# Kernel tuning notes

Hardware: AMD Instinct MI355X
Metric: run time of the kernel (lower is better)

## Reference

```python
import jax, jax.numpy as jnp
import numpy as np

B, H, W, C, NH, WS, NB = 8, 64, 64, 384, 12, 8, 2
N = H * W
NWT = WS * WS  # tokens per window
SHIFT = WS // 2

def _rel_index(ws):
    coords = np.stack(np.meshgrid(np.arange(ws), np.arange(ws), indexing='ij')).reshape(2, -1)
    rel = (coords[:, :, None] - coords[:, None, :]).transpose(1, 2, 0)
    rel[..., 0] += ws - 1
    rel[..., 1] += ws - 1
    rel[..., 0] *= 2 * ws - 1
    return rel.sum(-1)  # (ws*ws, ws*ws)

REL_IDX = _rel_index(WS)

def _shift_mask(h, w, ws, shift):
    img = np.zeros((h, w))
    cnt = 0
    for hs in (slice(0, -ws), slice(-ws, -shift), slice(-shift, None)):
        for wsl in (slice(0, -ws), slice(-ws, -shift), slice(-shift, None)):
            img[hs, wsl] = cnt
            cnt += 1
    win = img.reshape(h // ws, ws, w // ws, ws).transpose(0, 2, 1, 3).reshape(-1, ws * ws)
    diff = win[:, None, :] - win[:, :, None]
    return np.where(diff != 0, -100.0, 0.0).astype(np.float32)  # (nW, NWT, NWT)

MASK = jnp.asarray(_shift_mask(H, W, WS, SHIFT))

def _ln(x, g, b, eps=1e-5):
    m = jnp.mean(x, -1, keepdims=True)
    v = jnp.mean((x - m) ** 2, -1, keepdims=True)
    return (x - m) * jax.lax.rsqrt(v + eps) * g + b

def _partition(x):
    b = x.shape[0]
    x = x.reshape(b, H // WS, WS, W // WS, WS, C).transpose(0, 1, 3, 2, 4, 5)
    return x.reshape(-1, NWT, C)

def _reverse(wx, b):
    x = wx.reshape(b, H // WS, W // WS, WS, WS, C).transpose(0, 1, 3, 2, 4, 5)
    return x.reshape(b, H, W, C)

def _attention(xw, qkv_w, qkv_b, proj_w, proj_b, rpb, mask):
    B_, Nt, Cc = xw.shape
    hd = Cc // NH
    qkv = (xw @ qkv_w + qkv_b).reshape(B_, Nt, 3, NH, hd).transpose(2, 0, 3, 1, 4)
    q, k, v = qkv[0], qkv[1], qkv[2]
    bias = rpb[REL_IDX].transpose(2, 0, 1)[None]  # (1, NH, Nt, Nt)
    attn = jnp.einsum('bhnd,bhmd->bhnm', q * (hd ** -0.5), k) + bias
    if mask is not None:
        nW = mask.shape[0]
        attn = attn.reshape(B_ // nW, nW, NH, Nt, Nt) + mask[None, :, None]
        attn = attn.reshape(B_, NH, Nt, Nt)
    attn = jax.nn.softmax(attn, axis=-1)
    out = jnp.einsum('bhnm,bhmd->bhnd', attn, v).transpose(0, 2, 1, 3).reshape(B_, Nt, Cc)
    return out @ proj_w + proj_b

def _swin_block(x, p, shift):
    n1g, n1b, n2g, n2b, qw, qb, pw, pb, w1, b1, w2, b2, rpb = p
    shortcut = x
    h = _ln(x, n1g, n1b)
    if shift > 0:
        h = jnp.roll(h, (-shift, -shift), axis=(1, 2))
    hw = _attention(_partition(h), qw, qb, pw, pb, rpb, MASK if shift > 0 else None)
    h = _reverse(hw, x.shape[0])
    if shift > 0:
        h = jnp.roll(h, (shift, shift), axis=(1, 2))
    x = shortcut + h
    h = _ln(x, n2g, n2b)
    h = jax.nn.gelu(h @ w1 + b1) @ w2 + b2
    return x + h


def setup_inputs() -> dict:
    key = jax.random.key(0)
    ks = jax.random.split(key, 6)
    s = 0.02
    return {
        'x': jax.random.normal(ks[0], (B, N, C), jnp.float32),
        'outer_g': jnp.ones((NB, C), jnp.float32),
        'outer_b': jnp.zeros((NB, C), jnp.float32),
        'n1_g': jnp.ones((NB, C), jnp.float32),
        'n1_b': jnp.zeros((NB, C), jnp.float32),
        'n2_g': jnp.ones((NB, C), jnp.float32),
        'n2_b': jnp.zeros((NB, C), jnp.float32),
        'qkv_w': jax.random.normal(ks[1], (NB, C, 3 * C), jnp.float32) * s,
        'qkv_b': jnp.zeros((NB, 3 * C), jnp.float32),
        'proj_w': jax.random.normal(ks[2], (NB, C, C), jnp.float32) * s,
        'proj_b': jnp.zeros((NB, C), jnp.float32),
        'mlp_w1': jax.random.normal(ks[3], (NB, C, 4 * C), jnp.float32) * s,
        'mlp_b1': jnp.zeros((NB, 4 * C), jnp.float32),
        'mlp_w2': jax.random.normal(ks[4], (NB, 4 * C, C), jnp.float32) * s,
        'mlp_b2': jnp.zeros((NB, C), jnp.float32),
        'rpb': jax.random.normal(ks[5], (NB, (2 * WS - 1) ** 2, NH), jnp.float32) * s,
    }


def reference(x, outer_g, outer_b, n1_g, n1_b, n2_g, n2_b, qkv_w, qkv_b, proj_w, proj_b, mlp_w1, mlp_b1, mlp_w2, mlp_b2, rpb):
    xv = x.reshape(B, H, W, C)
    for i in range(NB):
        shift = 0 if i % 2 == 0 else SHIFT
        p = (n1_g[i], n1_b[i], n2_g[i], n2_b[i], qkv_w[i], qkv_b[i], proj_w[i], proj_b[i],
             mlp_w1[i], mlp_b1[i], mlp_w2[i], mlp_b2[i], rpb[i])
        residual = xv
        xv = _swin_block(_ln(xv, outer_g[i], outer_b[i]), p, shift) + residual
    return xv.reshape(B, N, C)
```

## Files before the change

### kernel.cpp

```cpp
#include <hip/hip_runtime.h>
#include <hip/hip_bf16.h>

#define BATCH 8
#define HDIM 64
#define WDIM 64
#define CC 384
#define NHE 12
#define HD 32
#define NTOK 32768
#define NBLK 2

typedef short short8 __attribute__((ext_vector_type(8)));
typedef float f32x4 __attribute__((ext_vector_type(4)));

__device__ __forceinline__ float bf2f(unsigned short u) {
  return __uint_as_float(((unsigned int)u) << 16);
}
__device__ __forceinline__ unsigned short f2bf(float f) {
  __hip_bfloat16 h = __float2bfloat16(f);
  return *reinterpret_cast<unsigned short*>(&h);
}
__device__ __forceinline__ float wave_sum(float s) {
#pragma unroll
  for (int o = 32; o; o >>= 1) s += __shfl_xor(s, o, 64);
  return s;
}
__device__ __forceinline__ float gelu_f(float x) {
  float y = 0.7978845608028654f * (x + 0.044715f * x * x * x);
  float t = 1.0f - 2.0f / (__expf(2.0f * y) + 1.0f);
  return 0.5f * x * (1.0f + t);
}
__device__ __forceinline__ int regid(int x) {
  return x < 56 ? 0 : (x < 60 ? 1 : 2);
}
__device__ __forceinline__ void gload16(const void* g, void* l) {
  __builtin_amdgcn_global_load_lds(
      (const __attribute__((address_space(1))) unsigned int*)g,
      (__attribute__((address_space(3))) unsigned int*)l, 16, 0, 0);
}

__global__ __launch_bounds__(256) void wconv_kernel(
    const float* __restrict__ src, unsigned short* __restrict__ dst, int K, int N) {
  __shared__ float tile[64 * 65];
  const int bn = blockIdx.x * 64, bk = blockIdx.y * 64;
  const int t = threadIdx.x;
  const int lk = t >> 2, ln = (t & 3) * 16;
  const float* ps = src + (size_t)(bk + lk) * N + bn + ln;
#pragma unroll
  for (int j = 0; j < 4; ++j)
    *(float4*)&tile[lk * 65 + ln + 4 * j] = *(const float4*)(ps + 4 * j);
  __syncthreads();
  const int on = t >> 2, ok = (t & 3) * 16;
  unsigned short ob[16];
#pragma unroll
  for (int j = 0; j < 16; ++j) ob[j] = f2bf(tile[(ok + j) * 65 + on]);
  uint4* pd = (uint4*)(dst + (size_t)(bn + on) * K + bk + ok);
  pd[0] = ((const uint4*)ob)[0];
  pd[1] = ((const uint4*)ob)[1];
}

__global__ __launch_bounds__(256) void bias_prep_kernel(
    const float* __restrict__ rpb, float* __restrict__ biasT) {
  int idx = blockIdx.x * 256 + threadIdx.x;
  int m = idx & 63;
  int n = (idx >> 6) & 63;
  int h = idx >> 12;
  int dr = (n >> 3) - (m >> 3) + 7;
  int dc = (n & 7) - (m & 7) + 7;
  biasT[idx] = rpb[(dr * 15 + dc) * NHE + h];
}

__global__ __launch_bounds__(256) void ln_fused_kernel(
    const float* __restrict__ xin, const float* __restrict__ og,
    const float* __restrict__ ob, const float* __restrict__ n1g,
    const float* __restrict__ n1b, unsigned short* __restrict__ y0h,
    unsigned short* __restrict__ abuf, int shift) {
  const int lane = threadIdx.x & 63;
  const int token = blockIdx.x * 4 + (threadIdx.x >> 6);
  const float* px = xin + (size_t)token * CC;
  float v[6];
#pragma unroll
  for (int j = 0; j < 6; ++j) v[j] = px[j * 64 + lane];
  float s = 0.f;
#pragma unroll
  for (int j = 0; j < 6; ++j) s += v[j];
  s = wave_sum(s);
  float mean = s * (1.0f / CC);
  float q = 0.f;
#pragma unroll
  for (int j = 0; j < 6; ++j) { float d = v[j] - mean; q += d * d; }
  q = wave_sum(q);
  float rstd = rsqrtf(q * (1.0f / CC) + 1e-5f);
  unsigned short* py = y0h + (size_t)token * CC;
#pragma unroll
  for (int j = 0; j < 6; ++j) {
    int d = j * 64 + lane;
    float y = (v[j] - mean) * rstd * og[d] + ob[d];
    py[d] = f2bf(y);
    v[j] = y;
  }
  s = 0.f;
#pragma unroll
  for (int j = 0; j < 6; ++j) s += v[j];
  s = wave_sum(s);
  float mean2 = s * (1.0f / CC);
  q = 0.f;
#pragma unroll
  for (int j = 0; j < 6; ++j) { float d = v[j] - mean2; q += d * d; }
  q = wave_sum(q);
  float rstd2 = rsqrtf(q * (1.0f / CC) + 1e-5f);
  int b = token >> 12;
  int hh = (token >> 6) & 63;
  int ww = token & 63;
  int r = (hh - shift) & 63;
  int c = (ww - shift) & 63;
  int wrow = (((b << 6) + ((r >> 3) << 3) + (c >> 3)) << 6) + ((r & 7) << 3) + (c & 7);
  unsigned short* pa = abuf + (size_t)wrow * CC;
#pragma unroll
  for (int j = 0; j < 6; ++j) {
    int d = j * 64 + lane;
    pa[d] = f2bf((v[j] - mean2) * rstd2 * n1g[d] + n1b[d]);
  }
}

__global__ __launch_bounds__(256, 1) void apl_kernel(
    const unsigned short* __restrict__ qkv, const float* __restrict__ biasT,
    const unsigned short* __restrict__ y0h, const unsigned short* __restrict__ Btp,
    const float* __restrict__ pb, const float* __restrict__ g2,
    const float* __restrict__ b2, unsigned short* __restrict__ x1h,
    unsigned short* __restrict__ abuf, int shift) {
  __shared__ __align__(1024) char smem[65536];
  const int tid = threadIdx.x;
  const int wv = tid >> 6;
  const int lane = tid & 63;
  const int l0 = lane & 15;
  const int q = lane >> 4;
  const int wi = blockIdx.x;
  const int use_mask = (shift != 0);

  unsigned short* P16 = (unsigned short*)(smem + wv * 12288);
  unsigned short* Vt16 = (unsigned short*)(smem + wv * 12288 + 8192);
  float* Ol = (float*)(smem + wv * 12288);
  unsigned short* Obuf = (unsigned short*)(smem + 49152);

#define LDS_FENCE() asm volatile("s_waitcnt lgkmcnt(0)" ::: "memory")

  f32x4 pacc[4][6] = {};

  for (int p = 0; p < 3; ++p) {
    const int h = 4 * p + wv;
    const unsigned short* qbase = qkv + (size_t)(wi * 64) * 1152 + h * HD;
    short8 kf[4], qf[4];
#pragma unroll
    for (int mt = 0; mt < 4; ++mt)
      kf[mt] = *(const short8*)(qbase + (size_t)(16 * mt + l0) * 1152 + CC + 8 * q);
#pragma unroll
    for (int nt = 0; nt < 4; ++nt)
      qf[nt] = *(const short8*)(qbase + (size_t)(16 * nt + l0) * 1152 + 8 * q);

    f32x4 acc[4][4];
    const float* bh = biasT + h * 4096;
#pragma unroll
    for (int mt = 0; mt < 4; ++mt)
#pragma unroll
      for (int nt = 0; nt < 4; ++nt)
        acc[mt][nt] = *(const f32x4*)(bh + (l0 + 16 * nt) * 64 + 16 * mt + 4 * q);

    {
      unsigned short varr[32];
      const uint4* pv = (const uint4*)(qbase + (size_t)lane * 1152 + 2 * CC);
      uint4* t4 = (uint4*)varr;
      t4[0] = pv[0]; t4[1] = pv[1]; t4[2] = pv[2]; t4[3] = pv[3];
#pragma unroll
      for (int d = 0; d < 32; ++d)
        Vt16[d * 64 + 8 * ((lane >> 3) ^ (d & 7)) + (lane & 7)] = varr[d];
    }

    __builtin_amdgcn_s_setprio(1);
#pragma unroll
    for (int mt = 0; mt < 4; ++mt)
#pragma unroll
      for (int nt = 0; nt < 4; ++nt)
        acc[mt][nt] = __builtin_amdgcn_mfma_f32_16x16x32_bf16(kf[mt], qf[nt], acc[mt][nt], 0, 0, 0);
    __builtin_amdgcn_s_setprio(0);

    if (use_mask) {
      int wloc = wi & 63;
      int wy = (wloc >> 3) * 8, wx = (wloc & 7) * 8;
      int idn[4], idm[16];
#pragma unroll
      for (int nt = 0; nt < 4; ++nt) {
        int n = l0 + 16 * nt;
        idn[nt] = regid(wy + (n >> 3)) * 3 + regid(wx + (n & 7));
      }
#pragma unroll
      for (int mt = 0; mt < 4; ++mt)
#pragma unroll
        for (int r = 0; r < 4; ++r) {
          int m = 16 * mt + 4 * q + r;
          idm[mt * 4 + r] = regid(wy + (m >> 3)) * 3 + regid(wx + (m & 7));
        }
#pragma unroll
      for (int mt = 0; mt < 4; ++mt)
#pragma unroll
        for (int nt = 0; nt < 4; ++nt)
#pragma unroll
          for (int r = 0; r < 4; ++r)
            acc[mt][nt][r] += (idm[mt * 4 + r] == idn[nt]) ? 0.0f : -100.0f;
    }

    float inv[4];
#pragma unroll
    for (int nt = 0; nt < 4; ++nt) {
      float m0 = -1e30f;
#pragma unroll
      for (int mt = 0; mt < 4; ++mt)
#pragma unroll
        for (int r = 0; r < 4; ++r) m0 = fmaxf(m0, acc[mt][nt][r]);
      m0 = fmaxf(m0, __shfl_xor(m0, 16, 64));
      m0 = fmaxf(m0, __shfl_xor(m0, 32, 64));
      float s0 = 0.f;
#pragma unroll
      for (int mt = 0; mt < 4; ++mt)
#pragma unroll
        for (int r = 0; r < 4; ++r) {
          float e = __expf(acc[mt][nt][r] - m0);
          acc[mt][nt][r] = e;
          s0 += e;
        }
      s0 += __shfl_xor(s0, 16, 64);
      s0 += __shfl_xor(s0, 32, 64);
      inv[nt] = 1.0f / s0;
    }

#pragma unroll
    for (int mt = 0; mt < 4; ++mt)
#pragma unroll
      for (int nt = 0; nt < 4; ++nt) {
        unsigned int lo = (unsigned int)f2bf(acc[mt][nt][0] * inv[nt]) |
                          ((unsigned int)f2bf(acc[mt][nt][1] * inv[nt]) << 16);
        unsigned int hi = (unsigned int)f2bf(acc[mt][nt][2] * inv[nt]) |
                          ((unsigned int)f2bf(acc[mt][nt][3] * inv[nt]) << 16);
        unsigned int* dst = (unsigned int*)&P16[(l0 + 16 * nt) * 64 +
                                                8 * ((2 * mt + (q >> 1)) ^ (l0 & 7)) + 4 * (q & 1)];
        dst[0] = lo;
        dst[1] = hi;
      }
    LDS_FENCE();

    f32x4 oacc[4][2] = {};
    __builtin_amdgcn_s_setprio(1);
#pragma unroll
    for (int kt = 0; kt < 2; ++kt) {
      short8 pa[4], vb[2];
#pragma unroll
      for (int nt = 0; nt < 4; ++nt)
        pa[nt] = *(const short8*)&P16[(l0 + 16 * nt) * 64 + 8 * ((q + 4 * kt) ^ (l0 & 7))];
#pragma unroll
      for (int dt = 0; dt < 2; ++dt)
        vb[dt] = *(const short8*)&Vt16[(l0 + 16 * dt) * 64 + 8 * ((q + 4 * kt) ^ (l0 & 7))];
#pragma unroll
      for (int nt = 0; nt < 4; ++nt)
#pragma unroll
        for (int dt = 0; dt < 2; ++dt)
          oacc[nt][dt] = __builtin_amdgcn_mfma_f32_16x16x32_bf16(pa[nt], vb[dt], oacc[nt][dt], 0, 0, 0);
    }
    __builtin_amdgcn_s_setprio(0);
    LDS_FENCE();

#pragma unroll
    for (int nt = 0; nt < 4; ++nt)
#pragma unroll
      for (int dt = 0; dt < 2; ++dt)
#pragma unroll
        for (int r = 0; r < 4; ++r)
          Ol[(16 * nt + 4 * q + r) * 34 + l0 + 16 * dt] = oacc[nt][dt][r];
    LDS_FENCE();

    uint4 opack[4];
    int posv[4];
#pragma unroll
    for (int jj = 0; jj < 4; ++jj) {
      int c = 4 * wv + jj;
      posv[jj] = (c & 8) | ((c ^ lane) & 7);
      unsigned short tmp[8];
#pragma unroll
      for (int e = 0; e < 8; ++e) tmp[e] = f2bf(Ol[lane * 34 + jj * 8 + e]);
      opack[jj] = *(const uint4*)tmp;
    }
    __syncthreads();
#pragma unroll
    for (int jj = 0; jj < 4; ++jj)
      *(uint4*)&Obuf[lane * 128 + posv[jj] * 8] = opack[jj];
    __syncthreads();

#pragma unroll
    for (int kfl = 0; kfl < 4; ++kfl) {
      short8 a[4], b[6];
      int c2 = kfl * 4 + q;
      int pos2 = (c2 & 8) | ((c2 ^ l0) & 7);
#pragma unroll
      for (int mt = 0; mt < 4; ++mt)
        a[mt] = *(const short8*)&Obuf[(16 * mt + l0) * 128 + pos2 * 8];
#pragma unroll
      for (int nt = 0; nt < 6; ++nt)
        b[nt] = *(const short8*)(Btp + (size_t)(wv * 96 + nt * 16 + l0) * 384 +
                                 128 * p + 32 * kfl + 8 * q);
      __builtin_amdgcn_s_setprio(1);
#pragma unroll
      for (int mt = 0; mt < 4; ++mt)
#pragma unroll
        for (int nt = 0; nt < 6; ++nt)
          pacc[mt][nt] = __builtin_amdgcn_mfma_f32_16x16x32_bf16(a[mt], b[nt], pacc[mt][nt], 0, 0, 0);
      __builtin_amdgcn_s_setprio(0);
    }
  }
  __syncthreads();

  float pbv[6], g2v[6], b2v[6];
#pragma unroll
  for (int nt = 0; nt < 6; ++nt) {
    int col = wv * 96 + nt * 16 + l0;
    pbv[nt] = pb[col];
    g2v[nt] = g2[col];
    b2v[nt] = b2[col];
  }
  int dstrow[4][4];
#pragma unroll
  for (int mt = 0; mt < 4; ++mt)
#pragma unroll
    for (int rr = 0; rr < 4; ++rr) {
      int m = 16 * mt + 4 * q + rr;
      int grow = wi * 64 + m;
      int b_ = grow >> 12;
      int wl = (grow >> 6) & 63;
      int t = grow & 63;
      int rs = ((wl >> 3) << 3) + (t >> 3);
      int cs = ((wl & 7) << 3) + (t & 7);
      int hh = (rs + shift) & 63;
      int ww = (cs + shift) & 63;
      dstrow[mt][rr] = (((b_ << 6) + hh) << 6) + ww;
    }
#pragma unroll
  for (int mt = 0; mt < 4; ++mt)
#pragma unroll
    for (int nt = 0; nt < 6; ++nt)
#pragma unroll
      for (int rr = 0; rr < 4; ++rr) {
        size_t dst = (size_t)dstrow[mt][rr] * CC + wv * 96 + nt * 16 + l0;
        pacc[mt][nt][rr] += pbv[nt] + bf2f(y0h[dst]);
      }
  float* part = (float*)(smem + 49152);
  float* stats = (float*)(smem + 49152 + 2048);
#pragma unroll
  for (int mt = 0; mt < 4; ++mt)
#pragma unroll
    for (int rr = 0; rr < 4; ++rr) {
      float s = 0.f, ss = 0.f;
#pragma unroll
      for (int nt = 0; nt < 6; ++nt) {
        float v = pacc[mt][nt][rr];
        s += v;
        ss += v * v;
      }
#pragma unroll
      for (int o = 8; o; o >>= 1) {
        s += __shfl_xor(s, o, 64);
        ss += __shfl_xor(ss, o, 64);
      }
      if (l0 == 0) {
        int m = 16 * mt + 4 * q + rr;
        part[(m * 4 + wv) * 2] = s;
        part[(m * 4 + wv) * 2 + 1] = ss;
      }
    }
  __syncthreads();
  if (tid < 64) {
    float s = 0.f, ss = 0.f;
#pragma unroll
    for (int w = 0; w < 4; ++w) {
      s += part[(tid * 4 + w) * 2];
      ss += part[(tid * 4 + w) * 2 + 1];
    }
    float mean = s * (1.0f / CC);
    float var = ss * (1.0f / CC) - mean * mean;
    stats[tid * 2] = mean;
    stats[tid * 2 + 1] = rsqrtf(var + 1e-5f);
  }
  __syncthreads();
#pragma unroll
  for (int mt = 0; mt < 4; ++mt)
#pragma unroll
    for (int rr = 0; rr < 4; ++rr) {
      int m = 16 * mt + 4 * q + rr;
      float mean = stats[m * 2];
      float rstd = stats[m * 2 + 1];
#pragma unroll
      for (int nt = 0; nt < 6; ++nt) {
        float v = pacc[mt][nt][rr];
        size_t dst = (size_t)dstrow[mt][rr] * CC + wv * 96 + nt * 16 + l0;
        x1h[dst] = f2bf(v);
        abuf[dst] = f2bf((v - mean) * rstd * g2v[nt] + b2v[nt]);
      }
    }
#undef LDS_FENCE
}

template <int EPI, int NN, int KK>
__global__ __launch_bounds__(256, 2) void gemm_kernel(
    const unsigned short* __restrict__ A, const unsigned short* __restrict__ Bt,
    const float* __restrict__ bias, float* __restrict__ outf,
    unsigned short* __restrict__ outb, const unsigned short* __restrict__ add0h,
    const float* __restrict__ add1f) {
  __shared__ __align__(1024) char smem[65536];
  const int tid = threadIdx.x;
  const int lane = tid & 63;
  const int wv = tid >> 6;
  const int wm = wv & 1, wn = wv >> 1;
  const int rowBase = blockIdx.y * 128;
  const int colBase = blockIdx.x * 128;
  const int srow = lane >> 3;
  const int schunk = (lane & 7) ^ srow;
  const unsigned short* pA = A + (size_t)(rowBase + srow) * KK + 8 * schunk;
  const unsigned short* pB = Bt + (size_t)(colBase + srow) * KK + 8 * schunk;
  const int l0 = lane & 15;
  const int q = lane >> 4;
  f32x4 acc[4][4] = {};

#pragma unroll
  for (int i = 0; i < 4; ++i) {
    int c = i * 4 + wv;
    gload16(pA + (size_t)(8 * c) * KK, smem + c * 1024);
    gload16(pB + (size_t)(8 * c) * KK, smem + 16384 + c * 1024);
  }

#pragma unroll 2
  for (int k0 = 0; k0 < KK; k0 += 64) {
    const int cur = (k0 >> 6) & 1;
    char* curb = smem + cur * 32768;
    if (k0 + 64 < KK) {
      char* nxtb = smem + (cur ^ 1) * 32768;
#pragma unroll
      for (int i = 0; i < 4; ++i) {
        int c = i * 4 + wv;
        gload16(pA + (size_t)(8 * c) * KK + k0 + 64, nxtb + c * 1024);
        gload16(pB + (size_t)(8 * c) * KK + k0 + 64, nxtb + 16384 + c * 1024);
      }
      asm volatile("s_waitcnt vmcnt(8)" ::: "memory");
    } else {
      asm volatile("s_waitcnt vmcnt(0)" ::: "memory");
    }
    __builtin_amdgcn_s_barrier();
    const unsigned short* As = (const unsigned short*)curb;
    const unsigned short* Bs = (const unsigned short*)(curb + 16384);
#pragma unroll
    for (int ksub = 0; ksub < 2; ++ksub) {
      const int sc = ksub * 4 + q;
      short8 af[4], bfr[4];
#pragma unroll
      for (int im = 0; im < 4; ++im) {
        int r = wm * 64 + im * 16 + l0;
        af[im] = *(const short8*)&As[r * 64 + 8 * (sc ^ (r & 7))];
      }
#pragma unroll
      for (int in_ = 0; in_ < 4; ++in_) {
        int r = wn * 64 + in_ * 16 + l0;
        bfr[in_] = *(const short8*)&Bs[r * 64 + 8 * (sc ^ (r & 7))];
      }
      __builtin_amdgcn_s_setprio(1);
#pragma unroll
      for (int im = 0; im < 4; ++im)
#pragma unroll
        for (int in_ = 0; in_ < 4; ++in_)
          acc[im][in_] = __builtin_amdgcn_mfma_f32_16x16x32_bf16(
              af[im], bfr[in_], acc[im][in_], 0, 0, 0);
      __builtin_amdgcn_s_setprio(0);
    }
    __builtin_amdgcn_s_barrier();
  }
  const int quad = lane >> 4;
  const int lc = lane & 15;
#pragma unroll
  for (int im = 0; im < 4; ++im) {
    int rb = rowBase + wm * 64 + im * 16 + quad * 4;
#pragma unroll
    for (int in_ = 0; in_ < 4; ++in_) {
      int gcol = colBase + wn * 64 + in_ * 16 + lc;
      float bv = bias[gcol];
#pragma unroll
      for (int r = 0; r < 4; ++r) {
        int grow = rb + r;
        float v = acc[im][in_][r] + bv;
        if (EPI == 0) {
          if (gcol < CC) v *= 0.17677669529663687f;
          outb[(size_t)grow * NN + gcol] = f2bf(v);
        } else if (EPI == 1) {
          outb[(size_t)grow * NN + gcol] = f2bf(gelu_f(v));
        } else {
          size_t dst = (size_t)grow * CC + gcol;
          outf[dst] = bf2f(add0h[dst]) + add1f[dst] + v;
        }
      }
    }
  }
}

extern "C" void kernel_launch(void* const* d_in, const int* in_sizes, int n_in,
                              void* d_out, int out_size, void* d_ws, size_t ws_size,
                              hipStream_t stream) {
  const float* x    = (const float*)d_in[0];
  const float* og   = (const float*)d_in[1];
  const float* ob   = (const float*)d_in[2];
  const float* n1g  = (const float*)d_in[3];
  const float* n1b  = (const float*)d_in[4];
  const float* n2g  = (const float*)d_in[5];
  const float* n2b  = (const float*)d_in[6];
  const float* qkvw = (const float*)d_in[7];
  const float* qkvb = (const float*)d_in[8];
  const float* pw   = (const float*)d_in[9];
  const float* pb   = (const float*)d_in[10];
  const float* w1   = (const float*)d_in[11];
  const float* b1   = (const float*)d_in[12];
  const float* w2   = (const float*)d_in[13];
  const float* b2   = (const float*)d_in[14];
  const float* rpb  = (const float*)d_in[15];
  float* out = (float*)d_out;

  char* ws = (char*)d_ws;
  unsigned short* y0h   = (unsigned short*)(ws);
  unsigned short* x1h   = (unsigned short*)(ws + 25165824);
  unsigned short* a_bf  = (unsigned short*)(ws + 50331648);
  unsigned short* big_bf= (unsigned short*)(ws + 100663296);
  unsigned short* wt    = (unsigned short*)(ws + 201326592);
  float* biasT          = (float*)(ws + 100663296 + 75497472);

  for (int i = 0; i < NBLK; ++i) {
    unsigned short* wq = wt + (size_t)i * 1769472;
    wconv_kernel<<<dim3(18, 6), 256, 0, stream>>>(qkvw + (size_t)i * 442368, wq, 384, 1152);
    wconv_kernel<<<dim3(6, 6), 256, 0, stream>>>(pw + (size_t)i * 147456, wq + 442368, 384, 384);
    wconv_kernel<<<dim3(24, 6), 256, 0, stream>>>(w1 + (size_t)i * 589824, wq + 589824, 384, 1536);
    wconv_kernel<<<dim3(6, 24), 256, 0, stream>>>(w2 + (size_t)i * 589824, wq + 1179648, 1536, 384);
  }

  for (int i = 0; i < NBLK; ++i) {
    const float* xin = (i == 0) ? x : out;
    int shift = (i & 1) ? 4 : 0;
    unsigned short* wq = wt + (size_t)i * 1769472;
    ln_fused_kernel<<<8192, 256, 0, stream>>>(xin, og + i * 384, ob + i * 384,
                                              n1g + i * 384, n1b + i * 384, y0h, a_bf, shift);
    gemm_kernel<0, 1152, 384><<<dim3(9, 256), 256, 0, stream>>>(
        a_bf, wq, qkvb + i * 1152, nullptr, big_bf, nullptr, nullptr);
    bias_prep_kernel<<<192, 256, 0, stream>>>(rpb + i * 2700, biasT);
    apl_kernel<<<512, 256, 0, stream>>>(big_bf, biasT, y0h, wq + 442368,
                                        pb + i * 384, n2g + i * 384, n2b + i * 384,
                                        x1h, a_bf, shift);
    gemm_kernel<1, 1536, 384><<<dim3(12, 256), 256, 0, stream>>>(
        a_bf, wq + 589824, b1 + i * 1536, nullptr, big_bf, nullptr, nullptr);
    gemm_kernel<3, 384, 1536><<<dim3(3, 256), 256, 0, stream>>>(
        big_bf, wq + 1179648, b2 + i * 384, out, nullptr, x1h, xin);
  }
}
```

Measured before the change: 704.8 us.

## Merge weight conversion launches and prefetch next head's QKV in attention kernel

Replaces eight small weight-conversion launches with a single kernel that works out which matrix and tile each block handles. In the fused attention/projection kernel, K, Q and V fragments for the next head group are loaded into registers while the current one computes. Barriers become an explicit lgkmcnt wait plus s_barrier instead of __syncthreads. The aim is to hide global load latency and cut launch overhead, at the cost of extra register pressure that may lower occupancy.

```diff
diff --git a/kernel.cpp b/kernel.cpp
--- a/kernel.cpp
+++ b/kernel.cpp
@@ -39,18 +39,31 @@
       (__attribute__((address_space(3))) unsigned int*)l, 16, 0, 0);
 }
 
-__global__ __launch_bounds__(256) void wconv_kernel(
-    const float* __restrict__ src, unsigned short* __restrict__ dst, int K, int N) {
+__global__ __launch_bounds__(256) void wconv_all_kernel(
+    const float* __restrict__ qkvw, const float* __restrict__ pw,
+    const float* __restrict__ w1, const float* __restrict__ w2,
+    unsigned short* __restrict__ wt) {
+  int t = blockIdx.x;
+  const int i = t / 432;
+  t -= i * 432;
+  unsigned short* wq = wt + (size_t)i * 1769472;
+  const float* src;
+  unsigned short* dst;
+  int K, N, nx;
+  if (t < 108)      { src = qkvw + (size_t)i * 442368; dst = wq;           K = 384;  N = 1152; nx = 18; }
+  else if (t < 144) { t -= 108; src = pw + (size_t)i * 147456; dst = wq + 442368;  K = 384;  N = 384;  nx = 6; }
+  else if (t < 288) { t -= 144; src = w1 + (size_t)i * 589824; dst = wq + 589824;  K = 384;  N = 1536; nx = 24; }
+  else              { t -= 288; src = w2 + (size_t)i * 589824; dst = wq + 1179648; K = 1536; N = 384;  nx = 6; }
+  const int bn = (t % nx) * 64, bk = (t / nx) * 64;
   __shared__ float tile[64 * 65];
-  const int bn = blockIdx.x * 64, bk = blockIdx.y * 64;
-  const int t = threadIdx.x;
-  const int lk = t >> 2, ln = (t & 3) * 16;
+  const int tt = threadIdx.x;
+  const int lk = tt >> 2, ln = (tt & 3) * 16;
   const float* ps = src + (size_t)(bk + lk) * N + bn + ln;
 #pragma unroll
   for (int j = 0; j < 4; ++j)
     *(float4*)&tile[lk * 65 + ln + 4 * j] = *(const float4*)(ps + 4 * j);
   __syncthreads();
-  const int on = t >> 2, ok = (t & 3) * 16;
+  const int on = tt >> 2, ok = (tt & 3) * 16;
   unsigned short ob[16];
 #pragma unroll
   for (int j = 0; j < 16; ++j) ob[j] = f2bf(tile[(ok + j) * 65 + on]);
@@ -144,19 +157,34 @@
   unsigned short* Obuf = (unsigned short*)(smem + 49152);
 
 #define LDS_FENCE() asm volatile("s_waitcnt lgkmcnt(0)" ::: "memory")
+#define LDS_BARRIER() do { LDS_FENCE(); __builtin_amdgcn_s_barrier(); } while (0)
+
+#define LOADP(PP, KD, QD, VD)                                                          \
+  {                                                                                    \
+    const unsigned short* qb_ = qkv + (size_t)(wi * 64) * 1152 + (4 * (PP) + wv) * HD; \
+    _Pragma("unroll") for (int mt_ = 0; mt_ < 4; ++mt_)                                \
+        KD[mt_] = *(const short8*)(qb_ + (size_t)(16 * mt_ + l0) * 1152 + CC + 8 * q); \
+    _Pragma("unroll") for (int nt_ = 0; nt_ < 4; ++nt_)                                \
+        QD[nt_] = *(const short8*)(qb_ + (size_t)(16 * nt_ + l0) * 1152 + 8 * q);      \
+    const uint4* pv_ = (const uint4*)(qb_ + (size_t)lane * 1152 + 2 * CC);             \
+    VD[0] = pv_[0]; VD[1] = pv_[1]; VD[2] = pv_[2]; VD[3] = pv_[3];                    \
+  }
 
   f32x4 pacc[4][6] = {};
+
+  short8 kf[4], qf[4];
+  uint4 varr4[4];
+  LOADP(0, kf, qf, varr4);
 
   for (int p = 0; p < 3; ++p) {
     const int h = 4 * p + wv;
-    const unsigned short* qbase = qkv + (size_t)(wi * 64) * 1152 + h * HD;
-    short8 kf[4], qf[4];
-#pragma unroll
-    for (int mt = 0; mt < 4; ++mt)
-      kf[mt] = *(const short8*)(qbase + (size_t)(16 * mt + l0) * 1152 + CC + 8 * q);
-#pragma unroll
-    for (int nt = 0; nt < 4; ++nt)
-      qf[nt] = *(const short8*)(qbase + (size_t)(16 * nt + l0) * 1152 + 8 * q);
+
+    {
+      const unsigned short* varr = (const unsigned short*)varr4;
+#pragma unroll
+      for (int d = 0; d < 32; ++d)
+        Vt16[d * 64 + 8 * ((lane >> 3) ^ (d & 7)) + (lane & 7)] = varr[d];
+    }
 
     f32x4 acc[4][4];
     const float* bh = biasT + h * 4096;
@@ -166,15 +194,9 @@
       for (int nt = 0; nt < 4; ++nt)
         acc[mt][nt] = *(const f32x4*)(bh + (l0 + 16 * nt) * 64 + 16 * mt + 4 * q);
 
-    {
-      unsigned short varr[32];
-      const uint4* pv = (const uint4*)(qbase + (size_t)lane * 1152 + 2 * CC);
-      uint4* t4 = (uint4*)varr;
-      t4[0] = pv[0]; t4[1] = pv[1]; t4[2] = pv[2]; t4[3] = pv[3];
-#pragma unroll
-      for (int d = 0; d < 32; ++d)
-        Vt16[d * 64 + 8 * ((lane >> 3) ^ (d & 7)) + (lane & 7)] = varr[d];
-    }
+    short8 kfn[4], qfn[4];
+    uint4 varrn[4];
+    if (p < 2) { LOADP(p + 1, kfn, qfn, varrn); }
 
     __builtin_amdgcn_s_setprio(1);
 #pragma unroll
@@ -288,11 +310,11 @@
       for (int e = 0; e < 8; ++e) tmp[e] = f2bf(Ol[lane * 34 + jj * 8 + e]);
       opack[jj] = *(const uint4*)tmp;
     }
-    __syncthreads();
+    LDS_BARRIER();
 #pragma unroll
     for (int jj = 0; jj < 4; ++jj)
       *(uint4*)&Obuf[lane * 128 + posv[jj] * 8] = opack[jj];
-    __syncthreads();
+    LDS_BARRIER();
 
 #pragma unroll
     for (int kfl = 0; kfl < 4; ++kfl) {
@@ -314,8 +336,17 @@
           pacc[mt][nt] = __builtin_amdgcn_mfma_f32_16x16x32_bf16(a[mt], b[nt], pacc[mt][nt], 0, 0, 0);
       __builtin_amdgcn_s_setprio(0);
     }
-  }
-  __syncthreads();
+
+    if (p < 2) {
+#pragma unroll
+      for (int j = 0; j < 4; ++j) {
+        kf[j] = kfn[j];
+        qf[j] = qfn[j];
+        varr4[j] = varrn[j];
+      }
+    }
+  }
+  LDS_BARRIER();
 
   float pbv[6], g2v[6], b2v[6];
 #pragma unroll
@@ -374,7 +405,7 @@
         part[(m * 4 + wv) * 2 + 1] = ss;
       }
     }
-  __syncthreads();
+  LDS_BARRIER();
   if (tid < 64) {
     float s = 0.f, ss = 0.f;
 #pragma unroll
@@ -387,7 +418,7 @@
     stats[tid * 2] = mean;
     stats[tid * 2 + 1] = rsqrtf(var + 1e-5f);
   }
-  __syncthreads();
+  LDS_BARRIER();
 #pragma unroll
   for (int mt = 0; mt < 4; ++mt)
 #pragma unroll
@@ -403,6 +434,8 @@
         abuf[dst] = f2bf((v - mean) * rstd * g2v[nt] + b2v[nt]);
       }
     }
+#undef LOADP
+#undef LDS_BARRIER
 #undef LDS_FENCE
 }
 
@@ -534,13 +567,7 @@
   unsigned short* wt    = (unsigned short*)(ws + 201326592);
   float* biasT          = (float*)(ws + 100663296 + 75497472);
 
-  for (int i = 0; i < NBLK; ++i) {
-    unsigned short* wq = wt + (size_t)i * 1769472;
-    wconv_kernel<<<dim3(18, 6), 256, 0, stream>>>(qkvw + (size_t)i * 442368, wq, 384, 1152);
-    wconv_kernel<<<dim3(6, 6), 256, 0, stream>>>(pw + (size_t)i * 147456, wq + 442368, 384, 384);
-    wconv_kernel<<<dim3(24, 6), 256, 0, stream>>>(w1 + (size_t)i * 589824, wq + 589824, 384, 1536);
-    wconv_kernel<<<dim3(6, 24), 256, 0, stream>>>(w2 + (size_t)i * 589824, wq + 1179648, 1536, 384);
-  }
+  wconv_all_kernel<<<864, 256, 0, stream>>>(qkvw, pw, w1, w2, wt);
 
   for (int i = 0; i < NBLK; ++i) {
     const float* xin = (i == 0) ? x : out;
```

Result: no change. 702.8 us (-0.3%).
